# Optimization experiments

Measured on AMD Instinct MI355X. Metric: run time of the kernel, lower is better.

## Reference

```python
import jax, jax.numpy as jnp
import numpy as np

B, H, W, C = 16, 64, 64, 512
C2 = C // 2
LN_EPS = 1e-3  # Keras LayerNormalization default epsilon


def setup_inputs() -> dict:
    key = jax.random.key(0)
    ks = jax.random.split(key, 8)
    s = 0.02
    return {
        "x": jax.random.normal(ks[0], (B, H, W, C), dtype=jnp.float32),
        "ch_wv_w": jax.random.normal(ks[1], (C, C2), dtype=jnp.float32) * s,
        "ch_wv_b": jnp.zeros((C2,), jnp.float32),
        "ch_wq_w": jax.random.normal(ks[2], (C, 1), dtype=jnp.float32) * s,
        "ch_wq_b": jnp.zeros((1,), jnp.float32),
        "ch_wz_w": jax.random.normal(ks[3], (C2, C), dtype=jnp.float32) * s,
        "ch_wz_b": jnp.zeros((C,), jnp.float32),
        "ln_gamma": jnp.ones((C,), jnp.float32),
        "ln_beta": jnp.zeros((C,), jnp.float32),
        "sp_wv_w": jax.random.normal(ks[4], (C, C2), dtype=jnp.float32) * s,
        "sp_wv_b": jnp.zeros((C2,), jnp.float32),
        "sp_wq_w": jax.random.normal(ks[5], (C, C2), dtype=jnp.float32) * s,
        "sp_wq_b": jnp.zeros((C2,), jnp.float32),
    }


def reference(x, ch_wv_w, ch_wv_b, ch_wq_w, ch_wq_b, ch_wz_w, ch_wz_b,
              ln_gamma, ln_beta, sp_wv_w, sp_wv_b, sp_wq_w, sp_wq_b):
    b, h, w, c = x.shape
    n = h * w
    c2 = c // 2

    # ---- channel-only branch ----
    # 1x1 convs are pointwise GEMMs over the channel dim
    ch_wv = jnp.einsum('bhwc,cd->bhwd', x, ch_wv_w) + ch_wv_b      # (B,H,W,C/2)
    ch_wq = jnp.einsum('bhwc,co->bhwo', x, ch_wq_w) + ch_wq_b      # (B,H,W,1)
    ch_wv = ch_wv.reshape(b, n, c2)                                # (B,N,C/2)
    ch_wq = jax.nn.softmax(ch_wq.reshape(b, n, 1), axis=1)         # softmax over N
    ch_wz = jnp.einsum('bnd,bno->bd', ch_wv, ch_wq)                # (B,C/2)
    ch_wz = jnp.einsum('bd,dc->bc', ch_wz, ch_wz_w) + ch_wz_b      # (B,C)

    # LayerNorm over axes [1,2,3] of (B,1,1,C) == normalize over C
    mean = jnp.mean(ch_wz, axis=-1, keepdims=True)
    var = jnp.var(ch_wz, axis=-1, keepdims=True)
    ch_wz = (ch_wz - mean) * jax.lax.rsqrt(var + LN_EPS) * ln_gamma + ln_beta
    channel_weight = jax.nn.sigmoid(ch_wz)[:, None, None, :]       # (B,1,1,C)
    channel_out = channel_weight * x                               # (B,H,W,C)

    # ---- spatial-only branch ----
    sp_wv = jnp.einsum('bhwc,cd->bhwd', channel_out, sp_wv_w) + sp_wv_b  # (B,H,W,C/2)
    sp_wq = jnp.einsum('bhwc,cd->bhwd', channel_out, sp_wq_w) + sp_wq_b  # (B,H,W,C/2)
    sp_wq = jnp.mean(sp_wq, axis=(1, 2))                           # GAP -> (B,C/2)
    sp_wq = jax.nn.softmax(sp_wq, axis=-1)                         # softmax over C/2
    sp_wv = sp_wv.reshape(b, n, c2)                                # (B,N,C/2)
    sp_wz = jnp.einsum('bd,bnd->bn', sp_wq, sp_wv)                 # (B,N)
    spatial_weight = jax.nn.sigmoid(sp_wz).reshape(b, h, w, 1)     # (B,H,W,1)
    return spatial_weight * channel_out
```

## Files before the change

kernel.cpp:

```cpp
#include <hip/hip_runtime.h>
#include <math.h>

#define BB 16
#define NN 4096
#define CC 512
#define C2 256
#define CHUNKS 64
#define RPC (NN/CHUNKS)

__device__ __forceinline__ float sigmoidf_(float z){ return 1.0f/(1.0f + __expf(-z)); }
__device__ __forceinline__ float dot8_(float4 a0, float4 a1, float4 b0, float4 b1){
    return a0.x*b0.x + a0.y*b0.y + a0.z*b0.z + a0.w*b0.w
         + a1.x*b1.x + a1.y*b1.y + a1.z*b1.z + a1.w*b1.w;
}

__global__ __launch_bounds__(256) void k_stats(const float* __restrict__ x,
        const float* __restrict__ wq,
        float* __restrict__ part_w, float* __restrict__ part_g,
        float* __restrict__ part_d)
{
    const int b = blockIdx.x / CHUNKS;
    const int k = blockIdx.x % CHUNKS;
    const int t = threadIdx.x, lane = t & 63, wv = t >> 6;
    __shared__ float rw[4][CC];
    __shared__ float rg[4][CC];
    __shared__ float rd[4];
    const long base = ((long)b*NN + (long)k*RPC) * CC;

    float4 w0 = *(const float4*)(wq + lane*4);
    float4 w1 = *(const float4*)(wq + 256 + lane*4);
    float4 aw0={0,0,0,0}, aw1={0,0,0,0}, ag0={0,0,0,0}, ag1={0,0,0,0};
    float den = 0.f;

    for (int i = 0; i < RPC/4; ++i) {
        const int r = wv*(RPC/4) + i;
        const float* xr = x + base + (long)r*CC;
        float4 a0 = *(const float4*)(xr + lane*4);
        float4 a1 = *(const float4*)(xr + 256 + lane*4);
        float d = dot8_(a0, a1, w0, w1);
        #pragma unroll
        for (int off = 32; off; off >>= 1) d += __shfl_xor(d, off);
        const float e = __expf(d);
        den += e;
        aw0.x = fmaf(e,a0.x,aw0.x); aw0.y = fmaf(e,a0.y,aw0.y);
        aw0.z = fmaf(e,a0.z,aw0.z); aw0.w = fmaf(e,a0.w,aw0.w);
        aw1.x = fmaf(e,a1.x,aw1.x); aw1.y = fmaf(e,a1.y,aw1.y);
        aw1.z = fmaf(e,a1.z,aw1.z); aw1.w = fmaf(e,a1.w,aw1.w);
        ag0.x += a0.x; ag0.y += a0.y; ag0.z += a0.z; ag0.w += a0.w;
        ag1.x += a1.x; ag1.y += a1.y; ag1.z += a1.z; ag1.w += a1.w;
    }
    *(float4*)&rw[wv][lane*4]       = aw0;
    *(float4*)&rw[wv][256+lane*4]   = aw1;
    *(float4*)&rg[wv][lane*4]       = ag0;
    *(float4*)&rg[wv][256+lane*4]   = ag1;
    if (lane == 0) rd[wv] = den;
    __syncthreads();

    const long o = (long)(b*CHUNKS + k)*CC;
    float s0 = rw[0][t]+rw[1][t]+rw[2][t]+rw[3][t];
    float s1 = rw[0][t+256]+rw[1][t+256]+rw[2][t+256]+rw[3][t+256];
    float g0 = rg[0][t]+rg[1][t]+rg[2][t]+rg[3][t];
    float g1 = rg[0][t+256]+rg[1][t+256]+rg[2][t+256]+rg[3][t+256];
    part_w[o + t] = s0;  part_w[o + t + 256] = s1;
    part_g[o + t] = g0;  part_g[o + t + 256] = g1;
    if (t == 0) part_d[b*CHUNKS + k] = rd[0]+rd[1]+rd[2]+rd[3];
}

__global__ __launch_bounds__(512) void k_chain(
    const float* __restrict__ part_w, const float* __restrict__ part_g,
    const float* __restrict__ part_d,
    const float* __restrict__ Wv,  const float* __restrict__ bv,
    const float* __restrict__ Wz,  const float* __restrict__ bz,
    const float* __restrict__ lng, const float* __restrict__ lnb,
    const float* __restrict__ Wq,  const float* __restrict__ bq,
    const float* __restrict__ Wv2, const float* __restrict__ bv2,
    float* __restrict__ cw, float* __restrict__ veff, float* __restrict__ constb)
{
    const int b = blockIdx.x, t = threadIdx.x, lane = t & 63, w = t >> 6;
    __shared__ float s_a[CC];
    __shared__ float s_b[CC];
    __shared__ float s_c[CC];
    __shared__ float s_m[C2];
    __shared__ float s_r[16];

    {
        const float* pwp = part_w + (long)b*CHUNKS*CC + t;
        const float* pgp = part_g + (long)b*CHUNKS*CC + t;
        float pw = 0.f, pg = 0.f;
        #pragma unroll 8
        for (int k = 0; k < CHUNKS; ++k) { pw += pwp[(long)k*CC]; pg += pgp[(long)k*CC]; }
        const float* pd = part_d + b*CHUNKS;
        float den = 0.f;
        #pragma unroll 8
        for (int k = 0; k < CHUNKS; ++k) den += pd[k];
        s_a[t] = pw / den;
        s_b[t] = pg;
    }
    __syncthreads();

    {
        const int d = t & 255, ch = t >> 8;
        const float* wp = Wv + (long)(ch*256)*C2 + d;
        const float* xp = s_a + ch*256;
        float a0=0,a1=0,a2=0,a3=0;
        #pragma unroll 8
        for (int c = 0; c < 256; c += 4) {
            a0 = fmaf(xp[c+0], wp[(long)(c+0)*C2], a0);
            a1 = fmaf(xp[c+1], wp[(long)(c+1)*C2], a1);
            a2 = fmaf(xp[c+2], wp[(long)(c+2)*C2], a2);
            a3 = fmaf(xp[c+3], wp[(long)(c+3)*C2], a3);
        }
        s_c[t] = (a0+a1)+(a2+a3);
    }
    __syncthreads();
    if (t < 256) s_m[t] = s_c[t] + s_c[t+256] + bv[t];
    __syncthreads();

    float zt;
    {
        const float* wp = Wz + t;
        float a0=0,a1=0,a2=0,a3=0;
        #pragma unroll 8
        for (int d = 0; d < 256; d += 4) {
            a0 = fmaf(s_m[d+0], wp[(long)(d+0)*CC], a0);
            a1 = fmaf(s_m[d+1], wp[(long)(d+1)*CC], a1);
            a2 = fmaf(s_m[d+2], wp[(long)(d+2)*CC], a2);
            a3 = fmaf(s_m[d+3], wp[(long)(d+3)*CC], a3);
        }
        zt = (a0+a1)+(a2+a3) + bz[t];
    }

    {
        float sum = zt, sq = zt*zt;
        #pragma unroll
        for (int off = 32; off; off >>= 1) { sum += __shfl_xor(sum, off); sq += __shfl_xor(sq, off); }
        if (lane == 0) { s_r[w] = sum; s_r[8+w] = sq; }
        __syncthreads();
        sum = 0.f; sq = 0.f;
        #pragma unroll
        for (int i = 0; i < 8; ++i) { sum += s_r[i]; sq += s_r[8+i]; }
        const float mean = sum * (1.f/CC);
        const float var  = sq  * (1.f/CC) - mean*mean;
        const float rstd = rsqrtf(var + 1e-3f);
        const float cwt = sigmoidf_((zt - mean)*rstd*lng[t] + lnb[t]);
        cw[b*CC + t] = cwt;
        __syncthreads();
        s_c[t] = cwt;
        s_a[t] = cwt * s_b[t] * (1.f/NN);
    }
    __syncthreads();

    {
        const int d = t & 255, ch = t >> 8;
        const float* wp = Wq + (long)(ch*256)*C2 + d;
        const float* xp = s_a + ch*256;
        float a0=0,a1=0,a2=0,a3=0;
        #pragma unroll 8
        for (int c = 0; c < 256; c += 4) {
            a0 = fmaf(xp[c+0], wp[(long)(c+0)*C2], a0);
            a1 = fmaf(xp[c+1], wp[(long)(c+1)*C2], a1);
            a2 = fmaf(xp[c+2], wp[(long)(c+2)*C2], a2);
            a3 = fmaf(xp[c+3], wp[(long)(c+3)*C2], a3);
        }
        s_b[t] = (a0+a1)+(a2+a3);
    }
    __syncthreads();

    float qv = 0.f;
    if (t < 256) qv = s_b[t] + s_b[t+256] + bq[t];
    {
        float mx = (t < 256) ? qv : -3.4e38f;
        #pragma unroll
        for (int off = 32; off; off >>= 1) mx = fmaxf(mx, __shfl_xor(mx, off));
        if (lane == 0) s_r[w] = mx;
        __syncthreads();
        mx = s_r[0];
        #pragma unroll
        for (int i = 1; i < 8; ++i) mx = fmaxf(mx, s_r[i]);
        float e = (t < 256) ? __expf(qv - mx) : 0.f;
        float se = e;
        #pragma unroll
        for (int off = 32; off; off >>= 1) se += __shfl_xor(se, off);
        __syncthreads();
        if (lane == 0) s_r[8+w] = se;
        __syncthreads();
        se = 0.f;
        #pragma unroll
        for (int i = 0; i < 8; ++i) se += s_r[8+i];
        const float qn = e / se;
        float cb = (t < 256) ? qn * bv2[t] : 0.f;
        #pragma unroll
        for (int off = 32; off; off >>= 1) cb += __shfl_xor(cb, off);
        if (lane == 0) s_r[w] = cb;
        __syncthreads();
        if (t < 256) s_b[t] = qn;
        if (t == 0) {
            float c_ = 0.f;
            #pragma unroll
            for (int i = 0; i < 8; ++i) c_ += s_r[i];
            constb[b] = c_;
        }
    }
    __syncthreads();

    {
        const int sub = lane & 15;
        float4 q0 = *(const float4*)(s_b + sub*16 + 0);
        float4 q1 = *(const float4*)(s_b + sub*16 + 4);
        float4 q2 = *(const float4*)(s_b + sub*16 + 8);
        float4 q3 = *(const float4*)(s_b + sub*16 + 12);
        for (int it = 0; it < 16; ++it) {
            const int c = (it*8 + w)*4 + (lane >> 4);
            const float4* wr = (const float4*)(Wv2 + (long)c*C2) + sub*4;
            float4 w0_ = wr[0], w1_ = wr[1], w2_ = wr[2], w3_ = wr[3];
            float d = w0_.x*q0.x + w0_.y*q0.y + w0_.z*q0.z + w0_.w*q0.w
                    + w1_.x*q1.x + w1_.y*q1.y + w1_.z*q1.z + w1_.w*q1.w
                    + w2_.x*q2.x + w2_.y*q2.y + w2_.z*q2.z + w2_.w*q2.w
                    + w3_.x*q3.x + w3_.y*q3.y + w3_.z*q3.z + w3_.w*q3.w;
            #pragma unroll
            for (int off = 8; off; off >>= 1) d += __shfl_xor(d, off);
            if (sub == 0) veff[b*CC + c] = s_c[c] * d;
        }
    }
}

__global__ __launch_bounds__(256) void k_final(const float* __restrict__ x,
        const float* __restrict__ cw, const float* __restrict__ veff,
        const float* __restrict__ constb, float* __restrict__ out)
{
    const int lane = threadIdx.x & 63;
    const int wv   = threadIdx.x >> 6;
    const long row = (long)blockIdx.x * 4 + wv;
    const int b = (int)(row >> 12);
    const float* xr = x + row * CC;
    float4 a0 = *(const float4*)(xr + lane*4);
    float4 a1 = *(const float4*)(xr + 256 + lane*4);
    const float* vb = veff + b*CC;
    float4 v0 = *(const float4*)(vb + lane*4);
    float4 v1 = *(const float4*)(vb + 256 + lane*4);
    float d = dot8_(a0, a1, v0, v1);
    #pragma unroll
    for (int off = 32; off; off >>= 1) d += __shfl_xor(d, off);
    const float sw = sigmoidf_(d + constb[b]);
    const float* cb = cw + b*CC;
    float4 c0 = *(const float4*)(cb + lane*4);
    float4 c1 = *(const float4*)(cb + 256 + lane*4);
    float4 o0, o1;
    o0.x = sw*c0.x*a0.x; o0.y = sw*c0.y*a0.y; o0.z = sw*c0.z*a0.z; o0.w = sw*c0.w*a0.w;
    o1.x = sw*c1.x*a1.x; o1.y = sw*c1.y*a1.y; o1.z = sw*c1.z*a1.z; o1.w = sw*c1.w*a1.w;
    *(float4*)(out + row*CC + lane*4)       = o0;
    *(float4*)(out + row*CC + 256 + lane*4) = o1;
}

extern "C" void kernel_launch(void* const* d_in, const int* in_sizes, int n_in,
                              void* d_out, int out_size, void* d_ws, size_t ws_size,
                              hipStream_t stream)
{
    const float* x       = (const float*)d_in[0];
    const float* ch_wv_w = (const float*)d_in[1];
    const float* ch_wv_b = (const float*)d_in[2];
    const float* ch_wq_w = (const float*)d_in[3];
    const float* ch_wz_w = (const float*)d_in[5];
    const float* ch_wz_b = (const float*)d_in[6];
    const float* ln_g    = (const float*)d_in[7];
    const float* ln_b    = (const float*)d_in[8];
    const float* sp_wv_w = (const float*)d_in[9];
    const float* sp_wv_b = (const float*)d_in[10];
    const float* sp_wq_w = (const float*)d_in[11];
    const float* sp_wq_b = (const float*)d_in[12];
    float* out = (float*)d_out;

    float* ws = (float*)d_ws;
    float* part_w  = ws;
    float* part_g  = part_w + BB*CHUNKS*CC;
    float* part_d  = part_g + BB*CHUNKS*CC;
    float* cw      = part_d + BB*CHUNKS;
    float* veff    = cw + BB*CC;
    float* constb  = veff + BB*CC;

    k_stats<<<BB*CHUNKS, 256, 0, stream>>>(x, ch_wq_w, part_w, part_g, part_d);
    k_chain<<<BB,        512, 0, stream>>>(part_w, part_g, part_d,
                                           ch_wv_w, ch_wv_b, ch_wz_w, ch_wz_b,
                                           ln_g, ln_b, sp_wq_w, sp_wq_b, sp_wv_w, sp_wv_b,
                                           cw, veff, constb);
    k_final<<<BB*NN/4,   256, 0, stream>>>(x, cw, veff, constb, out);
}
```

Before: 97.02 us.

## Convert chain weights to bf16 in stats kernel, halve chunks, use nontemporal IO

Adds 64 extra blocks to the stats kernel that convert the four weight matrices to bf16 in workspace, so the single-block-per-batch chain kernel streams half the weight bytes. CHUNKS drops from 64 to 32, which halves the partial sums the chain kernel must reduce but lengthens each stats block. The chain kernel reads partials with nontemporal loads, and the final kernel writes output with nontemporal stores. The bf16 weights add rounding error to the matrix-vector steps, and the conversion is redone on every call.

```diff
diff --git a/kernel.cpp b/kernel.cpp
--- a/kernel.cpp
+++ b/kernel.cpp
@@ -5,23 +5,52 @@
 #define NN 4096
 #define CC 512
 #define C2 256
-#define CHUNKS 64
+#define CHUNKS 32
 #define RPC (NN/CHUNKS)
+#define NW (CC*C2)
+
+typedef float  f4v __attribute__((ext_vector_type(4)));
+typedef unsigned short ushort;
+typedef unsigned int   uint;
 
 __device__ __forceinline__ float sigmoidf_(float z){ return 1.0f/(1.0f + __expf(-z)); }
 __device__ __forceinline__ float dot8_(float4 a0, float4 a1, float4 b0, float4 b1){
     return a0.x*b0.x + a0.y*b0.y + a0.z*b0.z + a0.w*b0.w
          + a1.x*b1.x + a1.y*b1.y + a1.z*b1.z + a1.w*b1.w;
 }
+__device__ __forceinline__ float bf2f(ushort u){ return __uint_as_float(((uint)u) << 16); }
+__device__ __forceinline__ ushort f2bf(float f){
+    uint u = __float_as_uint(f);
+    return (ushort)((u + 0x7FFFu + ((u >> 16) & 1u)) >> 16);
+}
+__device__ __forceinline__ float2 bfpair(uint v){
+    return make_float2(__uint_as_float(v << 16), __uint_as_float(v & 0xFFFF0000u));
+}
 
 __global__ __launch_bounds__(256) void k_stats(const float* __restrict__ x,
         const float* __restrict__ wq,
+        const float* __restrict__ Wv, const float* __restrict__ Wz,
+        const float* __restrict__ Wq2, const float* __restrict__ Wv2,
         float* __restrict__ part_w, float* __restrict__ part_g,
-        float* __restrict__ part_d)
+        float* __restrict__ part_d, ushort* __restrict__ wbf)
 {
+    const int t = threadIdx.x, lane = t & 63, wv = t >> 6;
+
+    if (blockIdx.x >= BB*CHUNKS) {
+        const int idx = blockIdx.x - BB*CHUNKS;
+        const int mat = idx >> 4;
+        const float* src = (mat == 0) ? Wv : (mat == 1) ? Wz : (mat == 2) ? Wq2 : Wv2;
+        const int boff = (idx & 15) * 8192;
+        ushort* dst = wbf + (long)mat*NW + boff;
+        const float* s = src + boff;
+        #pragma unroll 8
+        for (int e = 0; e < 32; ++e)
+            dst[t + e*256] = f2bf(s[t + e*256]);
+        return;
+    }
+
     const int b = blockIdx.x / CHUNKS;
     const int k = blockIdx.x % CHUNKS;
-    const int t = threadIdx.x, lane = t & 63, wv = t >> 6;
     __shared__ float rw[4][CC];
     __shared__ float rg[4][CC];
     __shared__ float rd[4];
@@ -49,34 +78,35 @@
         ag0.x += a0.x; ag0.y += a0.y; ag0.z += a0.z; ag0.w += a0.w;
         ag1.x += a1.x; ag1.y += a1.y; ag1.z += a1.z; ag1.w += a1.w;
     }
-    *(float4*)&rw[wv][lane*4]       = aw0;
-    *(float4*)&rw[wv][256+lane*4]   = aw1;
-    *(float4*)&rg[wv][lane*4]       = ag0;
-    *(float4*)&rg[wv][256+lane*4]   = ag1;
+    *(float4*)&rw[wv][lane*4]     = aw0;
+    *(float4*)&rw[wv][256+lane*4] = aw1;
+    *(float4*)&rg[wv][lane*4]     = ag0;
+    *(float4*)&rg[wv][256+lane*4] = ag1;
     if (lane == 0) rd[wv] = den;
     __syncthreads();
 
     const long o = (long)(b*CHUNKS + k)*CC;
-    float s0 = rw[0][t]+rw[1][t]+rw[2][t]+rw[3][t];
-    float s1 = rw[0][t+256]+rw[1][t+256]+rw[2][t+256]+rw[3][t+256];
-    float g0 = rg[0][t]+rg[1][t]+rg[2][t]+rg[3][t];
-    float g1 = rg[0][t+256]+rg[1][t+256]+rg[2][t+256]+rg[3][t+256];
-    part_w[o + t] = s0;  part_w[o + t + 256] = s1;
-    part_g[o + t] = g0;  part_g[o + t + 256] = g1;
+    part_w[o + t]       = rw[0][t]+rw[1][t]+rw[2][t]+rw[3][t];
+    part_w[o + t + 256] = rw[0][t+256]+rw[1][t+256]+rw[2][t+256]+rw[3][t+256];
+    part_g[o + t]       = rg[0][t]+rg[1][t]+rg[2][t]+rg[3][t];
+    part_g[o + t + 256] = rg[0][t+256]+rg[1][t+256]+rg[2][t+256]+rg[3][t+256];
     if (t == 0) part_d[b*CHUNKS + k] = rd[0]+rd[1]+rd[2]+rd[3];
 }
 
 __global__ __launch_bounds__(512) void k_chain(
     const float* __restrict__ part_w, const float* __restrict__ part_g,
     const float* __restrict__ part_d,
-    const float* __restrict__ Wv,  const float* __restrict__ bv,
-    const float* __restrict__ Wz,  const float* __restrict__ bz,
+    const ushort* __restrict__ wbf,
+    const float* __restrict__ bv,  const float* __restrict__ bz,
     const float* __restrict__ lng, const float* __restrict__ lnb,
-    const float* __restrict__ Wq,  const float* __restrict__ bq,
-    const float* __restrict__ Wv2, const float* __restrict__ bv2,
+    const float* __restrict__ bq,  const float* __restrict__ bv2,
     float* __restrict__ cw, float* __restrict__ veff, float* __restrict__ constb)
 {
     const int b = blockIdx.x, t = threadIdx.x, lane = t & 63, w = t >> 6;
+    const ushort* Wvb  = wbf;
+    const ushort* Wzb  = wbf + NW;
+    const ushort* Wqb  = wbf + 2*NW;
+    const ushort* Wv2b = wbf + 3*NW;
     __shared__ float s_a[CC];
     __shared__ float s_b[CC];
     __shared__ float s_c[CC];
@@ -88,7 +118,10 @@
         const float* pgp = part_g + (long)b*CHUNKS*CC + t;
         float pw = 0.f, pg = 0.f;
         #pragma unroll 8
-        for (int k = 0; k < CHUNKS; ++k) { pw += pwp[(long)k*CC]; pg += pgp[(long)k*CC]; }
+        for (int k = 0; k < CHUNKS; ++k) {
+            pw += __builtin_nontemporal_load(pwp + (long)k*CC);
+            pg += __builtin_nontemporal_load(pgp + (long)k*CC);
+        }
         const float* pd = part_d + b*CHUNKS;
         float den = 0.f;
         #pragma unroll 8
@@ -100,15 +133,15 @@
 
     {
         const int d = t & 255, ch = t >> 8;
-        const float* wp = Wv + (long)(ch*256)*C2 + d;
+        const ushort* wp = Wvb + (long)(ch*256)*C2 + d;
         const float* xp = s_a + ch*256;
         float a0=0,a1=0,a2=0,a3=0;
         #pragma unroll 8
         for (int c = 0; c < 256; c += 4) {
-            a0 = fmaf(xp[c+0], wp[(long)(c+0)*C2], a0);
-            a1 = fmaf(xp[c+1], wp[(long)(c+1)*C2], a1);
-            a2 = fmaf(xp[c+2], wp[(long)(c+2)*C2], a2);
-            a3 = fmaf(xp[c+3], wp[(long)(c+3)*C2], a3);
+            a0 = fmaf(xp[c+0], bf2f(wp[(long)(c+0)*C2]), a0);
+            a1 = fmaf(xp[c+1], bf2f(wp[(long)(c+1)*C2]), a1);
+            a2 = fmaf(xp[c+2], bf2f(wp[(long)(c+2)*C2]), a2);
+            a3 = fmaf(xp[c+3], bf2f(wp[(long)(c+3)*C2]), a3);
         }
         s_c[t] = (a0+a1)+(a2+a3);
     }
@@ -118,14 +151,14 @@
 
     float zt;
     {
-        const float* wp = Wz + t;
+        const ushort* wp = Wzb + t;
         float a0=0,a1=0,a2=0,a3=0;
         #pragma unroll 8
         for (int d = 0; d < 256; d += 4) {
-            a0 = fmaf(s_m[d+0], wp[(long)(d+0)*CC], a0);
-            a1 = fmaf(s_m[d+1], wp[(long)(d+1)*CC], a1);
-            a2 = fmaf(s_m[d+2], wp[(long)(d+2)*CC], a2);
-            a3 = fmaf(s_m[d+3], wp[(long)(d+3)*CC], a3);
+            a0 = fmaf(s_m[d+0], bf2f(wp[(long)(d+0)*CC]), a0);
+            a1 = fmaf(s_m[d+1], bf2f(wp[(long)(d+1)*CC]), a1);
+            a2 = fmaf(s_m[d+2], bf2f(wp[(long)(d+2)*CC]), a2);
+            a3 = fmaf(s_m[d+3], bf2f(wp[(long)(d+3)*CC]), a3);
         }
         zt = (a0+a1)+(a2+a3) + bz[t];
     }
@@ -152,15 +185,15 @@
 
     {
         const int d = t & 255, ch = t >> 8;
-        const float* wp = Wq + (long)(ch*256)*C2 + d;
+        const ushort* wp = Wqb + (long)(ch*256)*C2 + d;
         const float* xp = s_a + ch*256;
         float a0=0,a1=0,a2=0,a3=0;
         #pragma unroll 8
         for (int c = 0; c < 256; c += 4) {
-            a0 = fmaf(xp[c+0], wp[(long)(c+0)*C2], a0);
-            a1 = fmaf(xp[c+1], wp[(long)(c+1)*C2], a1);
-            a2 = fmaf(xp[c+2], wp[(long)(c+2)*C2], a2);
-            a3 = fmaf(xp[c+3], wp[(long)(c+3)*C2], a3);
+            a0 = fmaf(xp[c+0], bf2f(wp[(long)(c+0)*C2]), a0);
+            a1 = fmaf(xp[c+1], bf2f(wp[(long)(c+1)*C2]), a1);
+            a2 = fmaf(xp[c+2], bf2f(wp[(long)(c+2)*C2]), a2);
+            a3 = fmaf(xp[c+3], bf2f(wp[(long)(c+3)*C2]), a3);
         }
         s_b[t] = (a0+a1)+(a2+a3);
     }
@@ -211,12 +244,18 @@
         float4 q3 = *(const float4*)(s_b + sub*16 + 12);
         for (int it = 0; it < 16; ++it) {
             const int c = (it*8 + w)*4 + (lane >> 4);
-            const float4* wr = (const float4*)(Wv2 + (long)c*C2) + sub*4;
-            float4 w0_ = wr[0], w1_ = wr[1], w2_ = wr[2], w3_ = wr[3];
-            float d = w0_.x*q0.x + w0_.y*q0.y + w0_.z*q0.z + w0_.w*q0.w
-                    + w1_.x*q1.x + w1_.y*q1.y + w1_.z*q1.z + w1_.w*q1.w
-                    + w2_.x*q2.x + w2_.y*q2.y + w2_.z*q2.z + w2_.w*q2.w
-                    + w3_.x*q3.x + w3_.y*q3.y + w3_.z*q3.z + w3_.w*q3.w;
+            const uint4* wr = (const uint4*)(Wv2b + (long)c*C2) + sub*2;
+            uint4 u0 = wr[0], u1 = wr[1];
+            float2 p;
+            float d = 0.f;
+            p = bfpair(u0.x); d += p.x*q0.x + p.y*q0.y;
+            p = bfpair(u0.y); d += p.x*q0.z + p.y*q0.w;
+            p = bfpair(u0.z); d += p.x*q1.x + p.y*q1.y;
+            p = bfpair(u0.w); d += p.x*q1.z + p.y*q1.w;
+            p = bfpair(u1.x); d += p.x*q2.x + p.y*q2.y;
+            p = bfpair(u1.y); d += p.x*q2.z + p.y*q2.w;
+            p = bfpair(u1.z); d += p.x*q3.x + p.y*q3.y;
+            p = bfpair(u1.w); d += p.x*q3.z + p.y*q3.w;
             #pragma unroll
             for (int off = 8; off; off >>= 1) d += __shfl_xor(d, off);
             if (sub == 0) veff[b*CC + c] = s_c[c] * d;
@@ -245,11 +284,10 @@
     const float* cb = cw + b*CC;
     float4 c0 = *(const float4*)(cb + lane*4);
     float4 c1 = *(const float4*)(cb + 256 + lane*4);
-    float4 o0, o1;
-    o0.x = sw*c0.x*a0.x; o0.y = sw*c0.y*a0.y; o0.z = sw*c0.z*a0.z; o0.w = sw*c0.w*a0.w;
-    o1.x = sw*c1.x*a1.x; o1.y = sw*c1.y*a1.y; o1.z = sw*c1.z*a1.z; o1.w = sw*c1.w*a1.w;
-    *(float4*)(out + row*CC + lane*4)       = o0;
-    *(float4*)(out + row*CC + 256 + lane*4) = o1;
+    f4v o0 = { sw*c0.x*a0.x, sw*c0.y*a0.y, sw*c0.z*a0.z, sw*c0.w*a0.w };
+    f4v o1 = { sw*c1.x*a1.x, sw*c1.y*a1.y, sw*c1.z*a1.z, sw*c1.w*a1.w };
+    __builtin_nontemporal_store(o0, (f4v*)(out + row*CC + lane*4));
+    __builtin_nontemporal_store(o1, (f4v*)(out + row*CC + 256 + lane*4));
 }
 
 extern "C" void kernel_launch(void* const* d_in, const int* in_sizes, int n_in,
@@ -277,11 +315,13 @@
     float* cw      = part_d + BB*CHUNKS;
     float* veff    = cw + BB*CC;
     float* constb  = veff + BB*CC;
-
-    k_stats<<<BB*CHUNKS, 256, 0, stream>>>(x, ch_wq_w, part_w, part_g, part_d);
-    k_chain<<<BB,        512, 0, stream>>>(part_w, part_g, part_d,
-                                           ch_wv_w, ch_wv_b, ch_wz_w, ch_wz_b,
-                                           ln_g, ln_b, sp_wq_w, sp_wq_b, sp_wv_w, sp_wv_b,
-                                           cw, veff, constb);
-    k_final<<<BB*NN/4,   256, 0, stream>>>(x, cw, veff, constb, out);
-}
+    ushort* wbf    = (ushort*)(constb + BB);
+
+    k_stats<<<BB*CHUNKS + 64, 256, 0, stream>>>(x, ch_wq_w,
+                                                ch_wv_w, ch_wz_w, sp_wq_w, sp_wv_w,
+                                                part_w, part_g, part_d, wbf);
+    k_chain<<<BB,  512, 0, stream>>>(part_w, part_g, part_d, wbf,
+                                     ch_wv_b, ch_wz_b, ln_g, ln_b, sp_wq_b, sp_wv_b,
+                                     cw, veff, constb);
+    k_final<<<BB*NN/4, 256, 0, stream>>>(x, cw, veff, constb, out);
+}
```

Result: no change. 95.35 us (-1.7%).
